# Optimization experiments

Hardware: AMD Instinct MI355X
Metric: run time of the kernel (lower is better)

Reference implementation:

```python
import jax, jax.numpy as jnp
import numpy as np

B, T, C = 16, 1023, 2048
N_LAYER, LAYER_ID = 24, 12


def setup_inputs() -> dict:
    key = jax.random.key(0)
    k0, k1, k2, k3, k4 = jax.random.split(key, 5)
    x = jax.random.normal(k0, (B, T, C), jnp.float32)
    # decay schedule exactly as in RWKV_TimeMix.__init__ (first_sa_layer_id = 1)
    f1 = 3.0 + (LAYER_ID - 1) / (N_LAYER - 2) * (1.2 - 3.0)
    f2 = 0.65 + (LAYER_ID - 1) / (N_LAYER - 2) * (0.4 - 0.65)
    h = np.arange(C, dtype=np.float64)
    decay_speed = np.power(f2, h / (C - 1) * 7) * f1
    time_decay = jnp.asarray(np.log(decay_speed), jnp.float32)          # [C]
    time_first = jnp.full((C,), float(np.log(0.3)), jnp.float32)        # [C]
    time_mix = jnp.concatenate([jnp.zeros((C // 2,), jnp.float32),
                                jnp.ones((C - C // 2,), jnp.float32)])  # [C]
    s = 0.02
    Wk = jax.random.normal(k1, (C, C), jnp.float32) * s
    Wv = jax.random.normal(k2, (C, C), jnp.float32) * s
    Wr = jax.random.normal(k3, (C, C), jnp.float32) * s
    Wo = jax.random.normal(k4, (C, C), jnp.float32) * s
    z = jnp.zeros((B, C), jnp.float32)
    return {"x": x, "time_decay": time_decay, "time_first": time_first,
            "time_mix": time_mix, "Wk": Wk, "Wv": Wv, "Wr": Wr, "Wo": Wo,
            "xx": z, "aa": z, "bb": z, "mm": z}


def reference(x, time_decay, time_first, time_mix, Wk, Wv, Wr, Wo, xx, aa, bb, mm):
    Bn, Tn, Cn = x.shape
    # time_shift: prepend carried last-token state xx, drop last
    x_shift = jnp.concatenate([xx[:, None, :], x[:, :-1, :]], axis=1)
    xm = x * time_mix + x_shift * (1.0 - time_mix)
    k = xm @ Wk.T                       # [B, T, C]
    v = xm @ Wv.T
    r = xm @ Wr.T
    # running-max renorm to the nearest power of two: ldexp(0.5, frexp(max_t k).exponent)
    kmax = jax.lax.stop_gradient(jnp.max(k, axis=1))   # [B, C], max over time
    _, expo = jnp.frexp(kmax)
    mm_new = jnp.ldexp(jnp.float32(0.5), expo)          # [B, C]
    k = jnp.exp(k - mm_new[:, None, :])
    kv = k * v
    # TimeX kernel weights: w[c, T-1-delta] = exp(-exp(time_decay[c]) * (delta-1)) = d**(delta-1),
    # w[c, T-1] = exp(time_first[c]); so wk[t] = e_first*k[t] + sum_{u<t} d^{t-1-u} k[u] -> linear scan
    d = jnp.exp(-jnp.exp(time_decay))                   # [C] per-channel decay (= w[...,-3])
    e_first = jnp.exp(time_first)                       # [C] (w[...,-1])
    rsf = jnp.exp(mm - mm_new)                          # rescale carried state to new renorm
    k_seq = jnp.concatenate([(bb * rsf)[:, None, :], k], axis=1)    # [B, T+1, C]
    kv_seq = jnp.concatenate([(aa * rsf)[:, None, :], kv], axis=1)  # [B, T+1, C]

    def step(carry, inp):
        Sk, Skv = carry
        kt, kvt = inp
        out = (e_first * kt + Sk, e_first * kvt + Skv)
        return (d * Sk + kt, d * Skv + kvt), out

    init = (jnp.zeros((Bn, Cn), x.dtype), jnp.zeros((Bn, Cn), x.dtype))
    seq = (jnp.swapaxes(k_seq, 0, 1), jnp.swapaxes(kv_seq, 0, 1))   # [T+1, B, C]
    _, (wk_s, wkv_s) = jax.lax.scan(step, init, seq)
    wk = jnp.swapaxes(wk_s[1:], 0, 1)     # drop state slot -> [B, T, C]
    wkv = jnp.swapaxes(wkv_s[1:], 0, 1)
    rwkv = jax.nn.sigmoid(r) * jnp.nan_to_num(wkv / wk)
    return rwkv @ Wo.T
```

## Files before the change

kernel.cpp:

```cpp
#include <hip/hip_runtime.h>
#include <hip/hip_bf16.h>
#include <math.h>
#include <float.h>

#define BB 16
#define TT 1023
#define CC 2048
#define M_ROWS (BB * TT)
#define MP 16384
#define N3 (3 * CC)
#define NCH 16
#define CHL 64

typedef __attribute__((ext_vector_type(8))) short bfrag;
typedef __attribute__((ext_vector_type(4))) float f32x4;
typedef __attribute__((ext_vector_type(4))) short short4v;

__device__ __forceinline__ void async16(const void* g, void* l) {
  __builtin_amdgcn_global_load_lds((const __attribute__((address_space(1))) void*)g,
                                   (__attribute__((address_space(3))) void*)l, 16, 0, 0);
}

__device__ __forceinline__ short bfb(float f) {
  __hip_bfloat16 h = __float2bfloat16(f);
  return *reinterpret_cast<short*>(&h);
}

__global__ void cast_weights(const float* __restrict__ Wk, const float* __restrict__ Wv,
                             const float* __restrict__ Wr, const float* __restrict__ Wo,
                             __hip_bfloat16* __restrict__ W3, __hip_bfloat16* __restrict__ WoB) {
  size_t i4 = (size_t)blockIdx.x * 256 + threadIdx.x;
  size_t i = i4 * 4;
  float4 a = *(const float4*)(Wk + i);
  float4 b = *(const float4*)(Wv + i);
  float4 c = *(const float4*)(Wr + i);
  float4 d = *(const float4*)(Wo + i);
  *(short4v*)((short*)W3 + i)              = short4v{bfb(a.x), bfb(a.y), bfb(a.z), bfb(a.w)};
  *(short4v*)((short*)W3 + i + CC * CC)    = short4v{bfb(b.x), bfb(b.y), bfb(b.z), bfb(b.w)};
  *(short4v*)((short*)W3 + i + 2 * CC * CC) = short4v{bfb(c.x), bfb(c.y), bfb(c.z), bfb(c.w)};
  *(short4v*)((short*)WoB + i)             = short4v{bfb(d.x), bfb(d.y), bfb(d.z), bfb(d.w)};
}

__global__ void build_xm(const float* __restrict__ x, const float* __restrict__ xx,
                         const float* __restrict__ tmix, __hip_bfloat16* __restrict__ xm) {
  int m = blockIdx.x;
  short* orow = (short*)xm + (size_t)m * CC;
  if (m >= M_ROWS) {
    for (int c = threadIdx.x; c < CC / 4; c += 256)
      ((short4v*)orow)[c] = short4v{0, 0, 0, 0};
    return;
  }
  int b = m / TT, t = m - b * TT;
  const float* xrow = x + (size_t)m * CC;
  const float* xprev = (t == 0) ? (xx + (size_t)b * CC) : (xrow - CC);
  for (int c = threadIdx.x; c < CC / 4; c += 256) {
    float4 xv = ((const float4*)xrow)[c];
    float4 pv = ((const float4*)xprev)[c];
    float4 tm = ((const float4*)tmix)[c];
    ((short4v*)orow)[c] = short4v{
        bfb(xv.x * tm.x + pv.x * (1.0f - tm.x)),
        bfb(xv.y * tm.y + pv.y * (1.0f - tm.y)),
        bfb(xv.z * tm.z + pv.z * (1.0f - tm.z)),
        bfb(xv.w * tm.w + pv.w * (1.0f - tm.w))};
  }
}

template <int MODE>
__global__ __launch_bounds__(512, 2)
void gemm256(const short* __restrict__ A, const short* __restrict__ Bw,
             float* __restrict__ outF, __hip_bfloat16* __restrict__ outV,
             __hip_bfloat16* __restrict__ outR) {
  __shared__ short lds[65536];

  const int lane = threadIdx.x & 63, wid = threadIdx.x >> 6;
  const int wr = wid >> 2, wc = wid & 3;

  const int nx = gridDim.x;
  const int nwg = nx * gridDim.y;
  const int bid = blockIdx.y * nx + blockIdx.x;
  const int q = nwg >> 3;
  const int swz = (bid & 7) * q + (bid >> 3);
  const int mBase = (swz / nx) * 256;
  const int nBase = (swz % nx) * 256;

  const int srow = lane >> 2;
  const int scol = (((lane & 3) ^ ((lane >> 3) & 3)) * 8);
  const int stgOff = wid * 1024 + lane * 8;
  const short* aSrcBase = A  + (size_t)(mBase + wid * 32 + srow) * CC + scol;
  const short* bSrcBase = Bw + (size_t)(nBase + wid * 32 + srow) * CC + scol;

  const int ldOff = (lane & 15) * 32 + (((lane >> 4) ^ ((lane >> 1) & 3)) * 8);

  const short* pA0 = lds + wr * 128 * 32 + ldOff;
  const short* pA1 = pA0 + 32768;
  const short* pB0 = lds + 16384 + wc * 64 * 32 + ldOff;
  const short* pB1 = pB0 + 32768;

  f32x4 acc[2][4][4] = {};
  bfrag bq[4];

#define RGNA(buf, kh) ((buf) * 32768 + (kh) * 8192)
#define RGNB(buf, kh) (16384 + (buf) * 32768 + (kh) * 8192)

#define STG_A(buf, kh, tk) do { \
    const short* _s = aSrcBase + ((tk) * 64 + (kh) * 32); \
    short* _d = lds + RGNA(buf, kh) + stgOff; \
    async16(_s, _d); async16(_s + (size_t)16 * CC, _d + 512); } while (0)

#define STG_B(buf, kh, tk) do { \
    const short* _s = bSrcBase + ((tk) * 64 + (kh) * 32); \
    short* _d = lds + RGNB(buf, kh) + stgOff; \
    async16(_s, _d); async16(_s + (size_t)16 * CC, _d + 512); } while (0)

#define VMN(n) asm volatile("s_waitcnt vmcnt(" #n ")" ::: "memory")

#define PH(pA, pB, kh, mh, STAGE, WAIT) do { \
    bfrag aq[4]; \
    if ((mh) == 0) { \
      _Pragma("unroll") \
      for (int n = 0; n < 4; ++n) \
        bq[n] = *(const bfrag*)(pB + (kh) * 8192 + n * 16 * 32); \
    } \
    _Pragma("unroll") \
    for (int f = 0; f < 4; ++f) \
      aq[f] = *(const bfrag*)(pA + (kh) * 8192 + ((mh) * 64 + f * 16) * 32); \
    STAGE; \
    __builtin_amdgcn_s_barrier(); \
    __builtin_amdgcn_s_setprio(1); \
    _Pragma("unroll") \
    for (int f = 0; f < 4; ++f) \
      _Pragma("unroll") \
      for (int n = 0; n < 4; ++n) \
        acc[mh][f][n] = __builtin_amdgcn_mfma_f32_16x16x32_bf16(aq[f], bq[n], acc[mh][f][n], 0, 0, 0); \
    __builtin_amdgcn_s_setprio(0); \
    WAIT; \
    __builtin_amdgcn_s_barrier(); } while (0)

  STG_A(0, 0, 0); STG_B(0, 0, 0);
  STG_A(0, 1, 0); STG_B(0, 1, 0);
  STG_A(1, 0, 1); STG_B(1, 0, 1);
  VMN(2);
  __builtin_amdgcn_s_barrier();

  for (int ti = 0; ti < 30; ti += 2) {
    PH(pA0, pB0, 0, 0, STG_A(1, 1, ti + 1), );
    PH(pA0, pB0, 0, 1, STG_B(1, 1, ti + 1), );
    PH(pA0, pB0, 1, 0, STG_A(0, 0, ti + 2), );
    PH(pA0, pB0, 1, 1, STG_B(0, 0, ti + 2), VMN(2));
    PH(pA1, pB1, 0, 0, STG_A(0, 1, ti + 2), );
    PH(pA1, pB1, 0, 1, STG_B(0, 1, ti + 2), );
    PH(pA1, pB1, 1, 0, STG_A(1, 0, ti + 3), );
    PH(pA1, pB1, 1, 1, STG_B(1, 0, ti + 3), VMN(2));
  }
  PH(pA0, pB0, 0, 0, STG_A(1, 1, 31), );
  PH(pA0, pB0, 0, 1, STG_B(1, 1, 31), );
  PH(pA0, pB0, 1, 0, , );
  PH(pA0, pB0, 1, 1, , VMN(2));
  PH(pA1, pB1, 0, 0, , );
  PH(pA1, pB1, 0, 1, , VMN(0));
  PH(pA1, pB1, 1, 0, , );
  PH(pA1, pB1, 1, 1, , );

#undef PH
#undef VMN
#undef STG_A
#undef STG_B
#undef RGNA
#undef RGNB

#pragma unroll
  for (int mh = 0; mh < 2; ++mh)
#pragma unroll
    for (int f = 0; f < 4; ++f) {
      const int row0 = mBase + wr * 128 + mh * 64 + f * 16 + (lane >> 4) * 4;
      const int col0 = nBase + wc * 64 + (lane & 15);
#pragma unroll
      for (int n = 0; n < 4; ++n) {
        const int col = col0 + n * 16;
#pragma unroll
        for (int rr = 0; rr < 4; ++rr) {
          const int row = row0 + rr;
          if (row < M_ROWS) {
            float val = acc[mh][f][n][rr];
            if constexpr (MODE == 0) {
              outF[(size_t)row * CC + col] = val;
            } else {
              if (col < CC)          outF[(size_t)row * CC + col] = val;
              else if (col < 2 * CC) outV[(size_t)row * CC + (col - CC)] = __float2bfloat16(val);
              else                   outR[(size_t)row * CC + (col - 2 * CC)] = __float2bfloat16(val);
            }
          }
        }
      }
    }
}

__global__ __launch_bounds__(1024)
void scan_fuse2(const float* __restrict__ kraw, const __hip_bfloat16* __restrict__ v,
                const __hip_bfloat16* __restrict__ r, const float* __restrict__ aa,
                const float* __restrict__ bb, const float* __restrict__ mm,
                const float* __restrict__ tdec, const float* __restrict__ tfir,
                __hip_bfloat16* __restrict__ rwkv) {
  __shared__ float sBk[NCH][64], sBkv[NCH][64], sSk[NCH][64], sSkv[NCH][64];

  const int lane = threadIdx.x & 63, wid = threadIdx.x >> 6;
  const int c = blockIdx.x * 64 + lane;
  const int b = blockIdx.y;
  const int i = b * CC + c;

  const float dexp = expf(tdec[c]);
  const float d    = expf(-dexp);
  const float ef   = expf(tfir[c]);

  const int t0 = wid * CHL;
  const int t1 = (t0 + CHL < TT) ? t0 + CHL : TT;
  const size_t base = (size_t)b * TT * CC + c;

  if (wid < NCH - 1) {
    float Bk = 0.0f, Bkv = 0.0f;
    size_t off = base + (size_t)t0 * CC;
#pragma unroll 4
    for (int t = t0; t < t1; ++t, off += CC) {
      float kk = expf(kraw[off]);
      float kv = kk * __bfloat162float(v[off]);
      Bk = d * Bk + kk;
      Bkv = d * Bkv + kv;
    }
    sBk[wid][lane] = Bk;
    sBkv[wid][lane] = Bkv;
  }
  __syncthreads();

  if (wid == 0) {
    const float d64 = expf(-dexp * (float)CHL);
    const float sc = expf(mm[i]);
    float S = bb[i] * sc, Sv = aa[i] * sc;
#pragma unroll
    for (int j = 0; j < NCH; ++j) {
      sSk[j][lane] = S;
      sSkv[j][lane] = Sv;
      if (j < NCH - 1) {
        S = d64 * S + sBk[j][lane];
        Sv = d64 * Sv + sBkv[j][lane];
      }
    }
  }
  __syncthreads();

  float S = sSk[wid][lane], Sv = sSkv[wid][lane];
  size_t off = base + (size_t)t0 * CC;
#pragma unroll 4
  for (int t = t0; t < t1; ++t, off += CC) {
    float kk = expf(kraw[off]);
    float vv = __bfloat162float(v[off]);
    float rv = __bfloat162float(r[off]);
    float kv = kk * vv;
    float wk = ef * kk + S;
    float wkv = ef * kv + Sv;
    S = d * S + kk;
    Sv = d * Sv + kv;
    float ratio = wkv / wk;
    if (isnan(ratio)) ratio = 0.0f;
    else if (isinf(ratio)) ratio = ratio > 0.0f ? FLT_MAX : -FLT_MAX;
    float sig = 1.0f / (1.0f + expf(-rv));
    rwkv[off] = __float2bfloat16(sig * ratio);
  }
}

extern "C" void kernel_launch(void* const* d_in, const int* in_sizes, int n_in,
                              void* d_out, int out_size, void* d_ws, size_t ws_size,
                              hipStream_t stream) {
  const float* x    = (const float*)d_in[0];
  const float* tdec = (const float*)d_in[1];
  const float* tfir = (const float*)d_in[2];
  const float* tmix = (const float*)d_in[3];
  const float* Wk   = (const float*)d_in[4];
  const float* Wv   = (const float*)d_in[5];
  const float* Wr   = (const float*)d_in[6];
  const float* Wo   = (const float*)d_in[7];
  const float* xx   = (const float*)d_in[8];
  const float* aa   = (const float*)d_in[9];
  const float* bb   = (const float*)d_in[10];
  const float* mm   = (const float*)d_in[11];

  char* ws = (char*)d_ws;
  size_t o = 0;
  __hip_bfloat16* W3  = (__hip_bfloat16*)(ws + o); o += (size_t)N3 * CC * 2;
  __hip_bfloat16* WoB = (__hip_bfloat16*)(ws + o); o += (size_t)CC * CC * 2;
  __hip_bfloat16* xmB = (__hip_bfloat16*)(ws + o); o += (size_t)MP * CC * 2;
  __hip_bfloat16* vB  = (__hip_bfloat16*)(ws + o); o += (size_t)MP * CC * 2;
  __hip_bfloat16* rB  = (__hip_bfloat16*)(ws + o); o += (size_t)MP * CC * 2;

  float* kraw = (float*)d_out;
  __hip_bfloat16* rwkvB = xmB;

  cast_weights<<<CC * CC / 1024, 256, 0, stream>>>(Wk, Wv, Wr, Wo, W3, WoB);
  build_xm<<<MP, 256, 0, stream>>>(x, xx, tmix, xmB);
  gemm256<1><<<dim3(N3 / 256, MP / 256), 512, 0, stream>>>(
      (const short*)xmB, (const short*)W3, kraw, vB, rB);
  scan_fuse2<<<dim3(CC / 64, BB), 1024, 0, stream>>>(kraw, vB, rB, aa, bb, mm,
                                                     tdec, tfir, rwkvB);
  gemm256<0><<<dim3(CC / 256, MP / 256), 512, 0, stream>>>(
      (const short*)rwkvB, (const short*)WoB, (float*)d_out, nullptr, nullptr);
}
```

Before: 701.2 us.

## Double-buffer LDS fragment reads across MFMA phases and store exp(k) as fp16

The GEMM main loop now prefetches the next phase's A/B fragments from LDS into a second register set while the current phase's MFMAs run, and drops the mid-phase barrier, moving the global staging after the math. Separately, the first GEMM's epilogue applies exp to k and stores it as fp16 instead of raw fp32. This halves the bytes the scan reads for k and removes the exp from both scan passes. The register double-buffering raises VGPR pressure under launch_bounds(512,2), and fp16 exp(k) can overflow or lose precision, since k is not renormalised by mm_new here.

Result: no change. 709.5 us (+1.2%).

```diff
diff --git a/kernel.cpp b/kernel.cpp
--- a/kernel.cpp
+++ b/kernel.cpp
@@ -1,5 +1,6 @@
 #include <hip/hip_runtime.h>
 #include <hip/hip_bf16.h>
+#include <hip/hip_fp16.h>
 #include <math.h>
 #include <float.h>
 
@@ -68,8 +69,8 @@
 template <int MODE>
 __global__ __launch_bounds__(512, 2)
 void gemm256(const short* __restrict__ A, const short* __restrict__ Bw,
-             float* __restrict__ outF, __hip_bfloat16* __restrict__ outV,
-             __hip_bfloat16* __restrict__ outR) {
+             float* __restrict__ outF, __half* __restrict__ outH,
+             __hip_bfloat16* __restrict__ outV, __hip_bfloat16* __restrict__ outR) {
   __shared__ short lds[65536];
 
   const int lane = threadIdx.x & 63, wid = threadIdx.x >> 6;
@@ -97,7 +98,7 @@
   const short* pB1 = pB0 + 32768;
 
   f32x4 acc[2][4][4] = {};
-  bfrag bq[4];
+  bfrag aqA[4], aqB[4], bqA[4], bqB[4];
 
 #define RGNA(buf, kh) ((buf) * 32768 + (kh) * 8192)
 #define RGNB(buf, kh) (16384 + (buf) * 32768 + (kh) * 8192)
@@ -114,25 +115,26 @@
 
 #define VMN(n) asm volatile("s_waitcnt vmcnt(" #n ")" ::: "memory")
 
-#define PH(pA, pB, kh, mh, STAGE, WAIT) do { \
-    bfrag aq[4]; \
-    if ((mh) == 0) { \
-      _Pragma("unroll") \
-      for (int n = 0; n < 4; ++n) \
-        bq[n] = *(const bfrag*)(pB + (kh) * 8192 + n * 16 * 32); \
-    } \
+#define PFA(dst, pA, kh, mh) \
     _Pragma("unroll") \
     for (int f = 0; f < 4; ++f) \
-      aq[f] = *(const bfrag*)(pA + (kh) * 8192 + ((mh) * 64 + f * 16) * 32); \
-    STAGE; \
-    __builtin_amdgcn_s_barrier(); \
+      dst[f] = *(const bfrag*)(pA + (kh) * 8192 + ((mh) * 64 + f * 16) * 32);
+
+#define PFB(dst, pB, kh) \
+    _Pragma("unroll") \
+    for (int n = 0; n < 4; ++n) \
+      dst[n] = *(const bfrag*)(pB + (kh) * 8192 + n * 16 * 32);
+
+#define PH(ai, AQ, BQ, PF, STAGE, WAIT) do { \
+    PF \
     __builtin_amdgcn_s_setprio(1); \
     _Pragma("unroll") \
     for (int f = 0; f < 4; ++f) \
       _Pragma("unroll") \
       for (int n = 0; n < 4; ++n) \
-        acc[mh][f][n] = __builtin_amdgcn_mfma_f32_16x16x32_bf16(aq[f], bq[n], acc[mh][f][n], 0, 0, 0); \
+        acc[ai][f][n] = __builtin_amdgcn_mfma_f32_16x16x32_bf16(AQ[f], BQ[n], acc[ai][f][n], 0, 0, 0); \
     __builtin_amdgcn_s_setprio(0); \
+    STAGE; \
     WAIT; \
     __builtin_amdgcn_s_barrier(); } while (0)
 
@@ -141,27 +143,39 @@
   STG_A(1, 0, 1); STG_B(1, 0, 1);
   VMN(2);
   __builtin_amdgcn_s_barrier();
+  PFA(aqA, pA0, 0, 0)
+  PFB(bqA, pB0, 0)
 
   for (int ti = 0; ti < 30; ti += 2) {
-    PH(pA0, pB0, 0, 0, STG_A(1, 1, ti + 1), );
-    PH(pA0, pB0, 0, 1, STG_B(1, 1, ti + 1), );
-    PH(pA0, pB0, 1, 0, STG_A(0, 0, ti + 2), );
-    PH(pA0, pB0, 1, 1, STG_B(0, 0, ti + 2), VMN(2));
-    PH(pA1, pB1, 0, 0, STG_A(0, 1, ti + 2), );
-    PH(pA1, pB1, 0, 1, STG_B(0, 1, ti + 2), );
-    PH(pA1, pB1, 1, 0, STG_A(1, 0, ti + 3), );
-    PH(pA1, pB1, 1, 1, STG_B(1, 0, ti + 3), VMN(2));
-  }
-  PH(pA0, pB0, 0, 0, STG_A(1, 1, 31), );
-  PH(pA0, pB0, 0, 1, STG_B(1, 1, 31), );
-  PH(pA0, pB0, 1, 0, , );
-  PH(pA0, pB0, 1, 1, , VMN(2));
-  PH(pA1, pB1, 0, 0, , );
-  PH(pA1, pB1, 0, 1, , VMN(0));
-  PH(pA1, pB1, 1, 0, , );
-  PH(pA1, pB1, 1, 1, , );
+    PH(0, aqA, bqA, PFA(aqB, pA0, 0, 1),                    STG_A(1, 1, ti + 1), VMN(2));
+    PH(1, aqB, bqA, PFA(aqA, pA0, 1, 0) PFB(bqB, pB0, 1),   STG_B(1, 1, ti + 1), );
+    PH(0, aqA, bqB, PFA(aqB, pA0, 1, 1),                    STG_A(0, 0, ti + 2), VMN(2));
+    PH(1, aqB, bqB, PFA(aqA, pA1, 0, 0) PFB(bqA, pB1, 0),   STG_B(0, 0, ti + 2), );
+    PH(0, aqA, bqA, PFA(aqB, pA1, 0, 1),                    STG_A(0, 1, ti + 2), VMN(2));
+    PH(1, aqB, bqA, PFA(aqA, pA1, 1, 0) PFB(bqB, pB1, 1),   STG_B(0, 1, ti + 2), );
+    PH(0, aqA, bqB, PFA(aqB, pA1, 1, 1),                    STG_A(1, 0, ti + 3), VMN(2));
+    PH(1, aqB, bqB, PFA(aqA, pA0, 0, 0) PFB(bqA, pB0, 0),   STG_B(1, 0, ti + 3), );
+  }
+  PH(0, aqA, bqA, PFA(aqB, pA0, 0, 1),                      STG_A(1, 1, 31), VMN(2));
+  PH(1, aqB, bqA, PFA(aqA, pA0, 1, 0) PFB(bqB, pB0, 1),     STG_B(1, 1, 31), );
+  PH(0, aqA, bqB, PFA(aqB, pA0, 1, 1),                      , VMN(2));
+  PH(1, aqB, bqB, PFA(aqA, pA1, 0, 0) PFB(bqA, pB1, 0),     , );
+  PH(0, aqA, bqA, PFA(aqB, pA1, 0, 1),                      , VMN(0));
+  PH(1, aqB, bqA, PFA(aqA, pA1, 1, 0) PFB(bqB, pB1, 1),     , );
+  PH(0, aqA, bqB, PFA(aqB, pA1, 1, 1),                      , );
+  {
+    __builtin_amdgcn_s_setprio(1);
+#pragma unroll
+    for (int f = 0; f < 4; ++f)
+#pragma unroll
+      for (int n = 0; n < 4; ++n)
+        acc[1][f][n] = __builtin_amdgcn_mfma_f32_16x16x32_bf16(aqB[f], bqB[n], acc[1][f][n], 0, 0, 0);
+    __builtin_amdgcn_s_setprio(0);
+  }
 
 #undef PH
+#undef PFA
+#undef PFB
 #undef VMN
 #undef STG_A
 #undef STG_B
@@ -185,7 +199,7 @@
             if constexpr (MODE == 0) {
               outF[(size_t)row * CC + col] = val;
             } else {
-              if (col < CC)          outF[(size_t)row * CC + col] = val;
+              if (col < CC)          outH[(size_t)row * CC + col] = __float2half(expf(val));
               else if (col < 2 * CC) outV[(size_t)row * CC + (col - CC)] = __float2bfloat16(val);
               else                   outR[(size_t)row * CC + (col - 2 * CC)] = __float2bfloat16(val);
             }
@@ -196,7 +210,7 @@
 }
 
 __global__ __launch_bounds__(1024)
-void scan_fuse2(const float* __restrict__ kraw, const __hip_bfloat16* __restrict__ v,
+void scan_fuse2(const __half* __restrict__ ek, const __hip_bfloat16* __restrict__ v,
                 const __hip_bfloat16* __restrict__ r, const float* __restrict__ aa,
                 const float* __restrict__ bb, const float* __restrict__ mm,
                 const float* __restrict__ tdec, const float* __restrict__ tfir,
@@ -221,7 +235,7 @@
     size_t off = base + (size_t)t0 * CC;
 #pragma unroll 4
     for (int t = t0; t < t1; ++t, off += CC) {
-      float kk = expf(kraw[off]);
+      float kk = __half2float(ek[off]);
       float kv = kk * __bfloat162float(v[off]);
       Bk = d * Bk + kk;
       Bkv = d * Bkv + kv;
@@ -251,7 +265,7 @@
   size_t off = base + (size_t)t0 * CC;
 #pragma unroll 4
   for (int t = t0; t < t1; ++t, off += CC) {
-    float kk = expf(kraw[off]);
+    float kk = __half2float(ek[off]);
     float vv = __bfloat162float(v[off]);
     float rv = __bfloat162float(r[off]);
     float kv = kk * vv;
@@ -291,15 +305,15 @@
   __hip_bfloat16* vB  = (__hip_bfloat16*)(ws + o); o += (size_t)MP * CC * 2;
   __hip_bfloat16* rB  = (__hip_bfloat16*)(ws + o); o += (size_t)MP * CC * 2;
 
-  float* kraw = (float*)d_out;
+  __half* ekH = (__half*)d_out;
   __hip_bfloat16* rwkvB = xmB;
 
   cast_weights<<<CC * CC / 1024, 256, 0, stream>>>(Wk, Wv, Wr, Wo, W3, WoB);
   build_xm<<<MP, 256, 0, stream>>>(x, xx, tmix, xmB);
   gemm256<1><<<dim3(N3 / 256, MP / 256), 512, 0, stream>>>(
-      (const short*)xmB, (const short*)W3, kraw, vB, rB);
-  scan_fuse2<<<dim3(CC / 64, BB), 1024, 0, stream>>>(kraw, vB, rB, aa, bb, mm,
+      (const short*)xmB, (const short*)W3, nullptr, ekH, vB, rB);
+  scan_fuse2<<<dim3(CC / 64, BB), 1024, 0, stream>>>(ekH, vB, rB, aa, bb, mm,
                                                      tdec, tfir, rwkvB);
   gemm256<0><<<dim3(CC / 256, MP / 256), 512, 0, stream>>>(
-      (const short*)rwkvB, (const short*)WoB, (float*)d_out, nullptr, nullptr);
-}
+      (const short*)rwkvB, (const short*)WoB, (float*)d_out, nullptr, nullptr, nullptr);
+}
```
